# Performance work log

Hardware: AMD Instinct MI355X
Metric: run time of the kernel (lower is better)

The kernel has to match this reference:

```python
import jax, jax.numpy as jnp
import numpy as np

D_MODEL = 256
NUM_HEADS = 8
D_HEAD = D_MODEL // NUM_HEADS  # 32


def setup_inputs() -> dict:
    key = jax.random.key(0)
    ks = jax.random.split(key, 7)
    N, WH = 8, 2048
    s = 1.0 / np.sqrt(D_MODEL)
    return {
        "x": jax.random.normal(ks[0], (N, WH, D_MODEL), dtype=jnp.float32),
        "Wq": jax.random.normal(ks[1], (D_MODEL, D_MODEL), dtype=jnp.float32) * s,
        "bq": jnp.zeros((D_MODEL,), dtype=jnp.float32),
        "Wk": jax.random.normal(ks[2], (D_MODEL, D_MODEL), dtype=jnp.float32) * s,
        "bk": jnp.zeros((D_MODEL,), dtype=jnp.float32),
        "Wv": jax.random.normal(ks[3], (D_MODEL, D_MODEL), dtype=jnp.float32) * s,
        "bv": jnp.zeros((D_MODEL,), dtype=jnp.float32),
    }


def _mhsa(x, Wq, bq, Wk, bk, Wv, bv):
    N, WH, C = x.shape
    # QKV projections; reshape to (N, heads, WH, d_head)
    def split_heads(t):
        return t.reshape(N, WH, NUM_HEADS, D_HEAD).transpose(0, 2, 1, 3)
    Q = split_heads(x @ Wq + bq)
    K = split_heads(x @ Wk + bk)
    V = split_heads(x @ Wv + bv)
    # FAITHFUL to source: logits /= d_k**(-0.5)  ==  logits * sqrt(d_k)
    logits = jnp.einsum("nhqd,nhkd->nhqk", Q, K) * jnp.sqrt(jnp.float32(D_HEAD))
    attn = jax.nn.softmax(logits, axis=-1)  # dropout p=0.1 is identity in eval
    x_attn = jnp.einsum("nhqk,nhkd->nhqd", attn, V)
    x_attn = x_attn.transpose(0, 2, 1, 3).reshape(N, WH, C)
    # drop_path is identity in eval mode; residual add
    return x_attn + x


def reference(x, Wq, bq, Wk, bk, Wv, bv):
    return _mhsa(x, Wq, bq, Wk, bk, Wv, bv)
```

## Files before the change

### kernel.cpp

```cpp
#include <hip/hip_runtime.h>
#include <math.h>

#define WH 2048
#define DM 256
#define NHD 8
#define DH 32
#define NB 8

typedef __attribute__((ext_vector_type(8))) short short8;
typedef __attribute__((ext_vector_type(4))) short short4v;
typedef __attribute__((ext_vector_type(4))) float f32x4;

__device__ __forceinline__ unsigned short bf16_rn(float f) {
    unsigned u = __float_as_uint(f);
    return (unsigned short)((u + 0x8000u) >> 16);
}
__device__ __forceinline__ float bf16_to_f(unsigned short h) {
    return __uint_as_float(((unsigned)h) << 16);
}
__device__ __forceinline__ unsigned pack_bf16_rn(float f1, float f0) {
    return __builtin_amdgcn_perm(__float_as_uint(f1) + 0x8000u,
                                 __float_as_uint(f0) + 0x8000u, 0x07060302);
}
__device__ __forceinline__ void glds16(const void* g, void* l) {
    __builtin_amdgcn_global_load_lds(
        (const __attribute__((address_space(1))) unsigned int*)g,
        (__attribute__((address_space(3))) unsigned int*)l, 16, 0, 0);
}

__global__ __launch_bounds__(256) void xprep(
    const float* __restrict__ X,
    unsigned short* __restrict__ Xhi, unsigned short* __restrict__ Xlo)
{
    const size_t i = ((size_t)blockIdx.x * 256 + threadIdx.x) * 8;
    float4 a = *(const float4*)&X[i];
    float4 b = *(const float4*)&X[i + 4];
    float v[8] = {a.x, a.y, a.z, a.w, b.x, b.y, b.z, b.w};
    short8 hi, lo;
    #pragma unroll
    for (int e = 0; e < 8; e++) {
        unsigned short hb = bf16_rn(v[e]);
        hi[e] = (short)hb;
        lo[e] = (short)bf16_rn(v[e] - bf16_to_f(hb));
    }
    *(short8*)&Xhi[i] = hi;
    *(short8*)&Xlo[i] = lo;
}

__global__ __launch_bounds__(256) void wprep(
    const float* __restrict__ Wq, const float* __restrict__ Wk,
    const float* __restrict__ Wv,
    unsigned short* __restrict__ WThi, unsigned short* __restrict__ WTlo)
{
    const int z = blockIdx.y;
    const float* W = (z == 0) ? Wq : ((z == 1) ? Wk : Wv);
    const size_t zoff = (size_t)z * DM * DM;
    const int tg = blockIdx.x * 256 + threadIdx.x;
    #pragma unroll
    for (int j = 0; j < 4; j++) {
        const int f = tg + j * 4096;
        const int k  = f >> 6;
        const int n0 = (f & 63) * 4;
        float4 v = *(const float4*)&W[(size_t)k * DM + n0];
        float vv[4] = {v.x, v.y, v.z, v.w};
        #pragma unroll
        for (int i = 0; i < 4; i++) {
            unsigned short hb = bf16_rn(vv[i]);
            WThi[zoff + (size_t)(n0 + i) * DM + k] = hb;
            WTlo[zoff + (size_t)(n0 + i) * DM + k] = bf16_rn(vv[i] - bf16_to_f(hb));
        }
    }
}

__global__ __launch_bounds__(256, 1) void qkv_mfma(
    const unsigned short* __restrict__ Xhi, const unsigned short* __restrict__ Xlo,
    const unsigned short* __restrict__ WThi, const unsigned short* __restrict__ WTlo,
    const float* __restrict__ bq, const float* __restrict__ bk, const float* __restrict__ bv,
    unsigned short* __restrict__ Qhi, unsigned short* __restrict__ Qlo,
    unsigned short* __restrict__ Khi, unsigned short* __restrict__ Klo,
    unsigned short* __restrict__ Vt)
{
    __shared__ __align__(16) unsigned short arena[4 * 2 * 4096];

    const int z = blockIdx.z;
    const float* bias = (z == 0) ? bq : ((z == 1) ? bk : bv);
    const size_t zoff = (size_t)z * DM * DM;

    const int tid  = threadIdx.x;
    const int w    = tid >> 6;
    const int lane = tid & 63;
    const int col  = lane & 15;
    const int quad = lane >> 4;
    const int wr = w >> 1, wc = w & 1;
    const int bm = blockIdx.x * 128;
    const int bn = blockIdx.y * 128;

    const int perm16 = (((lane & 3) ^ ((lane >> 3) & 3))) * 16;
    const char* glane;
    if (w == 0)      glane = (const char*)Xhi + (size_t)(bm + (lane >> 2)) * 512 + perm16;
    else if (w == 1) glane = (const char*)Xlo + (size_t)(bm + (lane >> 2)) * 512 + perm16;
    else if (w == 2) glane = (const char*)(WThi + zoff) + (size_t)(bn + (lane >> 2)) * 512 + perm16;
    else             glane = (const char*)(WTlo + zoff) + (size_t)(bn + (lane >> 2)) * 512 + perm16;

    auto issue = [&](int kb, int b) {
        const char* g0 = glane + (size_t)kb * 64;
        unsigned short* l0 = &arena[w * 8192 + b * 4096];
        #pragma unroll
        for (int g = 0; g < 8; g++)
            glds16(g0 + (size_t)g * 8192, l0 + g * 512);
    };

    f32x4 acc[4][4];
    #pragma unroll
    for (int mi = 0; mi < 4; mi++)
        #pragma unroll
        for (int ni = 0; ni < 4; ni++) acc[mi][ni] = (f32x4){0.f, 0.f, 0.f, 0.f};

    const int sw = (col >> 1) & 3;
    const int fO = (quad ^ sw) * 8;

    issue(0, 0);
    __syncthreads();
    for (int kb = 0; kb < 8; kb++) {
        const int b = kb & 1;
        if (kb < 7) issue(kb + 1, b ^ 1);

        short8 ah[4], al[4], bh[4], bl[4];
        #pragma unroll
        for (int mi = 0; mi < 4; mi++) {
            const int ro = (wr * 64 + mi * 16 + col) * 32 + fO;
            ah[mi] = *(const short8*)&arena[        b * 4096 + ro];
            al[mi] = *(const short8*)&arena[ 8192 + b * 4096 + ro];
        }
        #pragma unroll
        for (int ni = 0; ni < 4; ni++) {
            const int no = (wc * 64 + ni * 16 + col) * 32 + fO;
            bh[ni] = *(const short8*)&arena[16384 + b * 4096 + no];
            bl[ni] = *(const short8*)&arena[24576 + b * 4096 + no];
        }
        #pragma unroll
        for (int mi = 0; mi < 4; mi++)
            #pragma unroll
            for (int ni = 0; ni < 4; ni++) {
                acc[mi][ni] = __builtin_amdgcn_mfma_f32_16x16x32_bf16(al[mi], bh[ni], acc[mi][ni], 0, 0, 0);
                acc[mi][ni] = __builtin_amdgcn_mfma_f32_16x16x32_bf16(ah[mi], bl[ni], acc[mi][ni], 0, 0, 0);
                acc[mi][ni] = __builtin_amdgcn_mfma_f32_16x16x32_bf16(ah[mi], bh[ni], acc[mi][ni], 0, 0, 0);
            }
        __syncthreads();
    }

    unsigned* Tp = (unsigned*)arena;
    const int n   = bm >> 11;
    const int wqb = bm & (WH - 1);
    const float qsc = (z == 0) ? 8.1611159f : 1.0f;

    #pragma unroll
    for (int p = 0; p < 2; p++) {
        if (wr == p) {
            #pragma unroll
            for (int mi = 0; mi < 4; mi++)
                #pragma unroll
                for (int ni = 0; ni < 4; ni++) {
                    const int lc = wc * 64 + ni * 16 + col;
                    const float bb = bias[bn + lc];
                    #pragma unroll
                    for (int r = 0; r < 4; r++) {
                        float v = (acc[mi][ni][r] + bb) * qsc;
                        unsigned short hb = bf16_rn(v);
                        unsigned short lb = bf16_rn(v - bf16_to_f(hb));
                        Tp[(mi * 16 + quad * 4 + r) * 132 + lc] =
                            (unsigned)hb | ((unsigned)lb << 16);
                    }
                }
        }
        __syncthreads();
        if (z == 2) {
            const int c = tid >> 1, half = tid & 1;
            const int coln = bn + c, h = coln >> 5, d = coln & 31;
            const int tI = (wqb + p * 64 + half * 32) >> 5;
            unsigned short* dst =
                &Vt[(((size_t)(n * NHD + h) * 64 + tI) * 32 + d) * 32];
            unsigned hi[16];
            #pragma unroll
            for (int jj = 0; jj < 16; jj++) {
                unsigned u0 = Tp[(half * 32 + 2 * jj    ) * 132 + c];
                unsigned u1 = Tp[(half * 32 + 2 * jj + 1) * 132 + c];
                hi[jj] = __builtin_amdgcn_perm(u1, u0, 0x05040100);
            }
            #pragma unroll
            for (int s = 0; s < 4; s++)
                *(uint4*)&dst[s * 8] = make_uint4(hi[4*s], hi[4*s+1], hi[4*s+2], hi[4*s+3]);
        } else {
            const int lr = tid >> 2, seg = tid & 3;
            const int coln0 = bn + seg * 32, h = coln0 >> 5;
            const size_t off = ((size_t)((n * NHD + h) * WH) + wqb + p * 64 + lr) * DH;
            unsigned short* Thi = (z == 0) ? Qhi : Khi;
            unsigned short* Tlo = (z == 0) ? Qlo : Klo;
            #pragma unroll
            for (int s = 0; s < 4; s++) {
                unsigned u[8], hi[4], lo[4];
                *(uint4*)&u[0] = *(uint4*)&Tp[lr * 132 + seg * 32 + s * 8];
                *(uint4*)&u[4] = *(uint4*)&Tp[lr * 132 + seg * 32 + s * 8 + 4];
                #pragma unroll
                for (int jj = 0; jj < 4; jj++) {
                    hi[jj] = __builtin_amdgcn_perm(u[2*jj+1], u[2*jj], 0x05040100);
                    lo[jj] = __builtin_amdgcn_perm(u[2*jj+1], u[2*jj], 0x07060302);
                }
                *(uint4*)&Thi[off + s * 8] = make_uint4(hi[0], hi[1], hi[2], hi[3]);
                *(uint4*)&Tlo[off + s * 8] = make_uint4(lo[0], lo[1], lo[2], lo[3]);
            }
        }
        __syncthreads();
    }
}

__global__ __launch_bounds__(256, 4) void attn(
    const unsigned short* __restrict__ Qhi, const unsigned short* __restrict__ Qlo,
    const unsigned short* __restrict__ Khi, const unsigned short* __restrict__ Klo,
    const unsigned short* __restrict__ Vt,  const float* __restrict__ X,
    float* __restrict__ Out)
{
    __shared__ __align__(16) unsigned short Kh[2][1024];
    __shared__ __align__(16) unsigned short Kl[2][1024];
    __shared__ __align__(16) unsigned short Vv[2][1024];

    const int tid  = threadIdx.x;
    const int w    = tid >> 6;
    const int lane = tid & 63;
    const int col  = lane & 15;
    const int quad = lane >> 4;
    const int nh   = blockIdx.y;
    const int q0   = blockIdx.x * 128;
    const size_t base = (size_t)nh * WH * DH;

    short8 qh[2], ql[2];
    #pragma unroll
    for (int f = 0; f < 2; f++) {
        const int qrow = q0 + f * 64 + w * 16 + col;
        qh[f] = *(const short8*)&Qhi[base + (size_t)qrow * DH + quad * 8];
        ql[f] = *(const short8*)&Qlo[base + (size_t)qrow * DH + quad * 8];
    }

    f32x4 ot00 = {0.f,0.f,0.f,0.f}, ot01 = {0.f,0.f,0.f,0.f};
    f32x4 ot10 = {0.f,0.f,0.f,0.f}, ot11 = {0.f,0.f,0.f,0.f};
    float mr0 = -INFINITY, mr1 = -INFINITY, lr0 = 0.f, lr1 = 0.f;

    const size_t toff = (size_t)(lane >> 2) * 64 + (((lane & 3) ^ ((lane >> 3) & 3))) * 16;
    const char* gb;
    unsigned short *ld0, *ld1;
    if (w == 0)      { gb = (const char*)(Khi + base);        ld0 = &Kh[0][0];   ld1 = &Kh[1][0];   }
    else if (w == 1) { gb = (const char*)(Klo + base);        ld0 = &Kl[0][0];   ld1 = &Kl[1][0];   }
    else if (w == 2) { gb = (const char*)(Vt  + base);        ld0 = &Vv[0][0];   ld1 = &Vv[1][0];   }
    else             { gb = (const char*)(Vt  + base) + 1024; ld0 = &Vv[0][512]; ld1 = &Vv[1][512]; }
    gb += toff;

    auto issue = [&](int t, unsigned short* ld) {
        const char* g = gb + (size_t)t * 2048;
        glds16(g, ld);
        if (w < 2) glds16(g + 1024, ld + 512);
    };

    const int sw  = (col >> 1) & 3;
    const int kO0 = col * 32 + (quad ^ sw) * 8;
    const int vO0 = col * 32 + ((quad >> 1) ^ sw) * 8 + (quad & 1) * 4;
    const int vO1 = col * 32 + ((2 + (quad >> 1)) ^ sw) * 8 + (quad & 1) * 4;

    auto body = [&](int b) {
        const short8 kh0 = *(const short8*)&Kh[b][kO0];
        const short8 kh1 = *(const short8*)&Kh[b][kO0 + 512];
        const short8 kl0 = *(const short8*)&Kl[b][kO0];
        const short8 kl1 = *(const short8*)&Kl[b][kO0 + 512];
        const short4v va00 = *(const short4v*)&Vv[b][vO0];
        const short4v va01 = *(const short4v*)&Vv[b][vO1];
        const short4v va10 = *(const short4v*)&Vv[b][vO0 + 512];
        const short4v va11 = *(const short4v*)&Vv[b][vO1 + 512];

        #pragma unroll
        for (int f = 0; f < 2; f++) {
            f32x4 s0 = {0.f,0.f,0.f,0.f}, s1 = {0.f,0.f,0.f,0.f};
            s0 = __builtin_amdgcn_mfma_f32_16x16x32_bf16(kh0, ql[f], s0, 0, 0, 0);
            s0 = __builtin_amdgcn_mfma_f32_16x16x32_bf16(kl0, qh[f], s0, 0, 0, 0);
            s0 = __builtin_amdgcn_mfma_f32_16x16x32_bf16(kh0, qh[f], s0, 0, 0, 0);
            s1 = __builtin_amdgcn_mfma_f32_16x16x32_bf16(kh1, ql[f], s1, 0, 0, 0);
            s1 = __builtin_amdgcn_mfma_f32_16x16x32_bf16(kl1, qh[f], s1, 0, 0, 0);
            s1 = __builtin_amdgcn_mfma_f32_16x16x32_bf16(kh1, qh[f], s1, 0, 0, 0);

            float mx = fmaxf(fmaxf(fmaxf(s0[0], s0[1]), fmaxf(s0[2], s0[3])),
                             fmaxf(fmaxf(s1[0], s1[1]), fmaxf(s1[2], s1[3])));
            mx = fmaxf(mx, __shfl_xor(mx, 16));
            mx = fmaxf(mx, __shfl_xor(mx, 32));
            float& mrf = f ? mr1 : mr0;
            float& lrf = f ? lr1 : lr0;
            const float mnew  = fmaxf(mrf, mx);
            const float alpha = __builtin_amdgcn_exp2f(mrf - mnew);

            float p0[4], p1[4], ps = 0.f;
            #pragma unroll
            for (int r = 0; r < 4; r++) {
                p0[r] = __builtin_amdgcn_exp2f(s0[r] - mnew); ps += p0[r];
                p1[r] = __builtin_amdgcn_exp2f(s1[r] - mnew); ps += p1[r];
            }
            ps += __shfl_xor(ps, 16);
            ps += __shfl_xor(ps, 32);
            lrf = lrf * alpha + ps;
            mrf = mnew;

            union { short4v v; unsigned u[2]; } Pb0, Pb1;
            Pb0.u[0] = pack_bf16_rn(p0[1], p0[0]);
            Pb0.u[1] = pack_bf16_rn(p0[3], p0[2]);
            Pb1.u[0] = pack_bf16_rn(p1[1], p1[0]);
            Pb1.u[1] = pack_bf16_rn(p1[3], p1[2]);

            f32x4& o0 = f ? ot10 : ot00;
            f32x4& o1 = f ? ot11 : ot01;
            #pragma unroll
            for (int r = 0; r < 4; r++) { o0[r] *= alpha; o1[r] *= alpha; }
            o0 = __builtin_amdgcn_mfma_f32_16x16x16bf16_1k(va00, Pb0.v, o0, 0, 0, 0);
            o0 = __builtin_amdgcn_mfma_f32_16x16x16bf16_1k(va01, Pb1.v, o0, 0, 0, 0);
            o1 = __builtin_amdgcn_mfma_f32_16x16x16bf16_1k(va10, Pb0.v, o1, 0, 0, 0);
            o1 = __builtin_amdgcn_mfma_f32_16x16x16bf16_1k(va11, Pb1.v, o1, 0, 0, 0);
        }
    };

    issue(0, ld0);
    __syncthreads();
    for (int kt2 = 0; kt2 < 32; kt2++) {
        issue(2 * kt2 + 1, ld1);
        body(0);
        __syncthreads();
        if (kt2 < 31) issue(2 * kt2 + 2, ld0);
        body(1);
        __syncthreads();
    }

    const int n = nh >> 3, h = nh & 7;
    #pragma unroll
    for (int f = 0; f < 2; f++) {
        const float inv = 1.f / (f ? lr1 : lr0);
        const f32x4& o0 = f ? ot10 : ot00;
        const f32x4& o1 = f ? ot11 : ot01;
        const int qrow = q0 + f * 64 + w * 16 + col;
        const size_t a0 = ((size_t)n * WH + qrow) * DM + h * DH + quad * 4;
        float4 x0 = *(const float4*)&X[a0];
        float4 y0;
        y0.x = o0[0] * inv + x0.x;
        y0.y = o0[1] * inv + x0.y;
        y0.z = o0[2] * inv + x0.z;
        y0.w = o0[3] * inv + x0.w;
        *(float4*)&Out[a0] = y0;
        float4 x1 = *(const float4*)&X[a0 + 16];
        float4 y1;
        y1.x = o1[0] * inv + x1.x;
        y1.y = o1[1] * inv + x1.y;
        y1.z = o1[2] * inv + x1.z;
        y1.w = o1[3] * inv + x1.w;
        *(float4*)&Out[a0 + 16] = y1;
    }
}

extern "C" void kernel_launch(void* const* d_in, const int* in_sizes, int n_in,
                              void* d_out, int out_size, void* d_ws, size_t ws_size,
                              hipStream_t stream) {
    const float* x  = (const float*)d_in[0];
    const float* Wq = (const float*)d_in[1];
    const float* bq = (const float*)d_in[2];
    const float* Wk = (const float*)d_in[3];
    const float* bk = (const float*)d_in[4];
    const float* Wv = (const float*)d_in[5];
    const float* bv = (const float*)d_in[6];
    float* out = (float*)d_out;

    const size_t elems = (size_t)NB * WH * DM;
    unsigned short* Qhi  = (unsigned short*)d_ws;
    unsigned short* Qlo  = Qhi + elems;
    unsigned short* Khi  = Qlo + elems;
    unsigned short* Klo  = Khi + elems;
    unsigned short* Vt   = Klo + elems;
    unsigned short* WThi = Vt  + elems;
    unsigned short* WTlo = WThi + (size_t)3 * DM * DM;

    unsigned short* Xhi = (unsigned short*)d_out;
    unsigned short* Xlo = Xhi + elems;

    xprep<<<2048, 256, 0, stream>>>(x, Xhi, Xlo);

    dim3 gw(16, 3);
    wprep<<<gw, 256, 0, stream>>>(Wq, Wk, Wv, WThi, WTlo);

    dim3 gg(128, 2, 3);
    qkv_mfma<<<gg, 256, 0, stream>>>(Xhi, Xlo, WThi, WTlo, bq, bk, bv,
                                     Qhi, Qlo, Khi, Klo, Vt);

    dim3 ga(WH / 128, NB * NHD);
    attn<<<ga, 256, 0, stream>>>(Qhi, Qlo, Khi, Klo, Vt, x, out);
}
```

Measured before the change: 232.6 us.

## Pack K/V tiles into contiguous blobs and process 64 keys per attention step

The QKV projection now writes K hi/lo and transposed V for each 64-key tile into one contiguous 12 KB blob per head, and X/W are pre-laid out in k-chunked blocks so GEMM tile loads are contiguous. The attention kernel loads each blob with three async LDS copies per wave and processes 64 keys per iteration instead of 32, halving loop iterations and barriers. Row-sum shuffles are deferred to the epilogue. In exchange it uses more LDS, holds more registers per iteration, and adds a new XOR swizzle for V reads.

```diff
diff --git a/kernel.cpp b/kernel.cpp
--- a/kernel.cpp
+++ b/kernel.cpp
@@ -33,6 +33,9 @@
     unsigned short* __restrict__ Xhi, unsigned short* __restrict__ Xlo)
 {
     const size_t i = ((size_t)blockIdx.x * 256 + threadIdx.x) * 8;
+    const int row = (int)(i >> 8);
+    const int k   = (int)(i & 255);
+    const size_t dst = ((size_t)(k >> 5) * 16384 + row) * 32 + (k & 31);
     float4 a = *(const float4*)&X[i];
     float4 b = *(const float4*)&X[i + 4];
     float v[8] = {a.x, a.y, a.z, a.w, b.x, b.y, b.z, b.w};
@@ -43,8 +46,8 @@
         hi[e] = (short)hb;
         lo[e] = (short)bf16_rn(v[e] - bf16_to_f(hb));
     }
-    *(short8*)&Xhi[i] = hi;
-    *(short8*)&Xlo[i] = lo;
+    *(short8*)&Xhi[dst] = hi;
+    *(short8*)&Xlo[dst] = lo;
 }
 
 __global__ __launch_bounds__(256) void wprep(
@@ -66,8 +69,9 @@
         #pragma unroll
         for (int i = 0; i < 4; i++) {
             unsigned short hb = bf16_rn(vv[i]);
-            WThi[zoff + (size_t)(n0 + i) * DM + k] = hb;
-            WTlo[zoff + (size_t)(n0 + i) * DM + k] = bf16_rn(vv[i] - bf16_to_f(hb));
+            const size_t dst = zoff + ((size_t)(k >> 5) * 256 + n0 + i) * 32 + (k & 31);
+            WThi[dst] = hb;
+            WTlo[dst] = bf16_rn(vv[i] - bf16_to_f(hb));
         }
     }
 }
@@ -77,8 +81,7 @@
     const unsigned short* __restrict__ WThi, const unsigned short* __restrict__ WTlo,
     const float* __restrict__ bq, const float* __restrict__ bk, const float* __restrict__ bv,
     unsigned short* __restrict__ Qhi, unsigned short* __restrict__ Qlo,
-    unsigned short* __restrict__ Khi, unsigned short* __restrict__ Klo,
-    unsigned short* __restrict__ Vt)
+    unsigned short* __restrict__ KV)
 {
     __shared__ __align__(16) unsigned short arena[4 * 2 * 4096];
 
@@ -96,18 +99,18 @@
     const int bn = blockIdx.y * 128;
 
     const int perm16 = (((lane & 3) ^ ((lane >> 3) & 3))) * 16;
-    const char* glane;
-    if (w == 0)      glane = (const char*)Xhi + (size_t)(bm + (lane >> 2)) * 512 + perm16;
-    else if (w == 1) glane = (const char*)Xlo + (size_t)(bm + (lane >> 2)) * 512 + perm16;
-    else if (w == 2) glane = (const char*)(WThi + zoff) + (size_t)(bn + (lane >> 2)) * 512 + perm16;
-    else             glane = (const char*)(WTlo + zoff) + (size_t)(bn + (lane >> 2)) * 512 + perm16;
+    const char* glane; size_t kstr;
+    if (w == 0)      { glane = (const char*)Xhi + (size_t)(bm + (lane >> 2)) * 64 + perm16; kstr = (size_t)16384 * 64; }
+    else if (w == 1) { glane = (const char*)Xlo + (size_t)(bm + (lane >> 2)) * 64 + perm16; kstr = (size_t)16384 * 64; }
+    else if (w == 2) { glane = (const char*)(WThi + zoff) + (size_t)(bn + (lane >> 2)) * 64 + perm16; kstr = 256 * 64; }
+    else             { glane = (const char*)(WTlo + zoff) + (size_t)(bn + (lane >> 2)) * 64 + perm16; kstr = 256 * 64; }
 
     auto issue = [&](int kb, int b) {
-        const char* g0 = glane + (size_t)kb * 64;
+        const char* g0 = glane + (size_t)kb * kstr;
         unsigned short* l0 = &arena[w * 8192 + b * 4096];
         #pragma unroll
         for (int g = 0; g < 8; g++)
-            glds16(g0 + (size_t)g * 8192, l0 + g * 512);
+            glds16(g0 + (size_t)g * 1024, l0 + g * 512);
     };
 
     f32x4 acc[4][4];
@@ -177,9 +180,10 @@
         if (z == 2) {
             const int c = tid >> 1, half = tid & 1;
             const int coln = bn + c, h = coln >> 5, d = coln & 31;
-            const int tI = (wqb + p * 64 + half * 32) >> 5;
+            const int key0 = wqb + p * 64 + half * 32;
+            const int t = key0 >> 6, k6 = key0 & 63;
             unsigned short* dst =
-                &Vt[(((size_t)(n * NHD + h) * 64 + tI) * 32 + d) * 32];
+                &KV[(((size_t)(n * NHD + h) * 32 + t) * 6144) + 4096 + d * 64 + k6];
             unsigned hi[16];
             #pragma unroll
             for (int jj = 0; jj < 16; jj++) {
@@ -190,12 +194,13 @@
             #pragma unroll
             for (int s = 0; s < 4; s++)
                 *(uint4*)&dst[s * 8] = make_uint4(hi[4*s], hi[4*s+1], hi[4*s+2], hi[4*s+3]);
-        } else {
+        } else if (z == 1) {
             const int lr = tid >> 2, seg = tid & 3;
-            const int coln0 = bn + seg * 32, h = coln0 >> 5;
-            const size_t off = ((size_t)((n * NHD + h) * WH) + wqb + p * 64 + lr) * DH;
-            unsigned short* Thi = (z == 0) ? Qhi : Khi;
-            unsigned short* Tlo = (z == 0) ? Qlo : Klo;
+            const int h = (bn + seg * 32) >> 5;
+            const int key = wqb + p * 64 + lr;
+            const int t = key >> 6, k6 = key & 63;
+            unsigned short* blobK =
+                &KV[(((size_t)(n * NHD + h) * 32 + t) * 6144) + k6 * 32];
             #pragma unroll
             for (int s = 0; s < 4; s++) {
                 unsigned u[8], hi[4], lo[4];
@@ -206,8 +211,25 @@
                     hi[jj] = __builtin_amdgcn_perm(u[2*jj+1], u[2*jj], 0x05040100);
                     lo[jj] = __builtin_amdgcn_perm(u[2*jj+1], u[2*jj], 0x07060302);
                 }
-                *(uint4*)&Thi[off + s * 8] = make_uint4(hi[0], hi[1], hi[2], hi[3]);
-                *(uint4*)&Tlo[off + s * 8] = make_uint4(lo[0], lo[1], lo[2], lo[3]);
+                *(uint4*)&blobK[s * 8]        = make_uint4(hi[0], hi[1], hi[2], hi[3]);
+                *(uint4*)&blobK[2048 + s * 8] = make_uint4(lo[0], lo[1], lo[2], lo[3]);
+            }
+        } else {
+            const int lr = tid >> 2, seg = tid & 3;
+            const int h = (bn + seg * 32) >> 5;
+            const size_t off = ((size_t)((n * NHD + h) * WH) + wqb + p * 64 + lr) * DH;
+            #pragma unroll
+            for (int s = 0; s < 4; s++) {
+                unsigned u[8], hi[4], lo[4];
+                *(uint4*)&u[0] = *(uint4*)&Tp[lr * 132 + seg * 32 + s * 8];
+                *(uint4*)&u[4] = *(uint4*)&Tp[lr * 132 + seg * 32 + s * 8 + 4];
+                #pragma unroll
+                for (int jj = 0; jj < 4; jj++) {
+                    hi[jj] = __builtin_amdgcn_perm(u[2*jj+1], u[2*jj], 0x05040100);
+                    lo[jj] = __builtin_amdgcn_perm(u[2*jj+1], u[2*jj], 0x07060302);
+                }
+                *(uint4*)&Qhi[off + s * 8] = make_uint4(hi[0], hi[1], hi[2], hi[3]);
+                *(uint4*)&Qlo[off + s * 8] = make_uint4(lo[0], lo[1], lo[2], lo[3]);
             }
         }
         __syncthreads();
@@ -216,13 +238,10 @@
 
 __global__ __launch_bounds__(256, 4) void attn(
     const unsigned short* __restrict__ Qhi, const unsigned short* __restrict__ Qlo,
-    const unsigned short* __restrict__ Khi, const unsigned short* __restrict__ Klo,
-    const unsigned short* __restrict__ Vt,  const float* __restrict__ X,
+    const unsigned short* __restrict__ KV,  const float* __restrict__ X,
     float* __restrict__ Out)
 {
-    __shared__ __align__(16) unsigned short Kh[2][1024];
-    __shared__ __align__(16) unsigned short Kl[2][1024];
-    __shared__ __align__(16) unsigned short Vv[2][1024];
+    __shared__ __align__(16) unsigned short B[2][6144];
 
     const int tid  = threadIdx.x;
     const int w    = tid >> 6;
@@ -231,62 +250,74 @@
     const int quad = lane >> 4;
     const int nh   = blockIdx.y;
     const int q0   = blockIdx.x * 128;
-    const size_t base = (size_t)nh * WH * DH;
+    const size_t qbase = (size_t)nh * WH * DH;
+    const char* blob = (const char*)(KV + (size_t)nh * 196608);
 
     short8 qh[2], ql[2];
     #pragma unroll
     for (int f = 0; f < 2; f++) {
         const int qrow = q0 + f * 64 + w * 16 + col;
-        qh[f] = *(const short8*)&Qhi[base + (size_t)qrow * DH + quad * 8];
-        ql[f] = *(const short8*)&Qlo[base + (size_t)qrow * DH + quad * 8];
-    }
-
-    f32x4 ot00 = {0.f,0.f,0.f,0.f}, ot01 = {0.f,0.f,0.f,0.f};
-    f32x4 ot10 = {0.f,0.f,0.f,0.f}, ot11 = {0.f,0.f,0.f,0.f};
+        qh[f] = *(const short8*)&Qhi[qbase + (size_t)qrow * DH + quad * 8];
+        ql[f] = *(const short8*)&Qlo[qbase + (size_t)qrow * DH + quad * 8];
+    }
+
+    f32x4 o00 = {0.f,0.f,0.f,0.f}, o01 = {0.f,0.f,0.f,0.f};
+    f32x4 o10 = {0.f,0.f,0.f,0.f}, o11 = {0.f,0.f,0.f,0.f};
     float mr0 = -INFINITY, mr1 = -INFINITY, lr0 = 0.f, lr1 = 0.f;
 
-    const size_t toff = (size_t)(lane >> 2) * 64 + (((lane & 3) ^ ((lane >> 3) & 3))) * 16;
-    const char* gb;
-    unsigned short *ld0, *ld1;
-    if (w == 0)      { gb = (const char*)(Khi + base);        ld0 = &Kh[0][0];   ld1 = &Kh[1][0];   }
-    else if (w == 1) { gb = (const char*)(Klo + base);        ld0 = &Kl[0][0];   ld1 = &Kl[1][0];   }
-    else if (w == 2) { gb = (const char*)(Vt  + base);        ld0 = &Vv[0][0];   ld1 = &Vv[1][0];   }
-    else             { gb = (const char*)(Vt  + base) + 1024; ld0 = &Vv[0][512]; ld1 = &Vv[1][512]; }
-    gb += toff;
-
-    auto issue = [&](int t, unsigned short* ld) {
-        const char* g = gb + (size_t)t * 2048;
-        glds16(g, ld);
-        if (w < 2) glds16(g + 1024, ld + 512);
+    const char* gseg[3];
+    int loseg[3];
+    #pragma unroll
+    for (int j = 0; j < 3; j++) {
+        const int s = w * 3 + j;
+        int loff;
+        if (s < 8) loff = (lane >> 2) * 64  + (((lane & 3) ^ ((lane >> 3) & 3)) << 4);
+        else       loff = (lane >> 3) * 128 + (((lane & 7) ^ ((lane >> 3) & 7)) << 4);
+        gseg[j] = blob + s * 1024 + loff;
+        loseg[j] = s * 512;
+    }
+
+    auto issue = [&](int t, int b) {
+        #pragma unroll
+        for (int j = 0; j < 3; j++)
+            glds16(gseg[j] + (size_t)t * 12288, &B[b][loseg[j]]);
     };
 
-    const int sw  = (col >> 1) & 3;
-    const int kO0 = col * 32 + (quad ^ sw) * 8;
-    const int vO0 = col * 32 + ((quad >> 1) ^ sw) * 8 + (quad & 1) * 4;
-    const int vO1 = col * 32 + ((2 + (quad >> 1)) ^ sw) * 8 + (quad & 1) * 4;
+    const int sw = (col >> 1) & 3;
 
     auto body = [&](int b) {
-        const short8 kh0 = *(const short8*)&Kh[b][kO0];
-        const short8 kh1 = *(const short8*)&Kh[b][kO0 + 512];
-        const short8 kl0 = *(const short8*)&Kl[b][kO0];
-        const short8 kl1 = *(const short8*)&Kl[b][kO0 + 512];
-        const short4v va00 = *(const short4v*)&Vv[b][vO0];
-        const short4v va01 = *(const short4v*)&Vv[b][vO1];
-        const short4v va10 = *(const short4v*)&Vv[b][vO0 + 512];
-        const short4v va11 = *(const short4v*)&Vv[b][vO1 + 512];
-
+        const unsigned short* Bp = &B[b][0];
+        short8 kh[4], kl[4];
+        #pragma unroll
+        for (int kc = 0; kc < 4; kc++) {
+            const int ro = (col + kc * 16) * 32 + (quad ^ sw) * 8;
+            kh[kc] = *(const short8*)&Bp[ro];
+            kl[kc] = *(const short8*)&Bp[2048 + ro];
+        }
+        short4v va[4][2];
+        #pragma unroll
+        for (int kc = 0; kc < 4; kc++) {
+            const int cl = kc * 2 + (quad >> 1);
+            const int co = ((cl ^ (col & 7)) << 3) + (quad & 1) * 4;
+            va[kc][0] = *(const short4v*)&Bp[4096 + (col     ) * 64 + co];
+            va[kc][1] = *(const short4v*)&Bp[4096 + (col + 16) * 64 + co];
+        }
         #pragma unroll
         for (int f = 0; f < 2; f++) {
-            f32x4 s0 = {0.f,0.f,0.f,0.f}, s1 = {0.f,0.f,0.f,0.f};
-            s0 = __builtin_amdgcn_mfma_f32_16x16x32_bf16(kh0, ql[f], s0, 0, 0, 0);
-            s0 = __builtin_amdgcn_mfma_f32_16x16x32_bf16(kl0, qh[f], s0, 0, 0, 0);
-            s0 = __builtin_amdgcn_mfma_f32_16x16x32_bf16(kh0, qh[f], s0, 0, 0, 0);
-            s1 = __builtin_amdgcn_mfma_f32_16x16x32_bf16(kh1, ql[f], s1, 0, 0, 0);
-            s1 = __builtin_amdgcn_mfma_f32_16x16x32_bf16(kl1, qh[f], s1, 0, 0, 0);
-            s1 = __builtin_amdgcn_mfma_f32_16x16x32_bf16(kh1, qh[f], s1, 0, 0, 0);
-
-            float mx = fmaxf(fmaxf(fmaxf(s0[0], s0[1]), fmaxf(s0[2], s0[3])),
-                             fmaxf(fmaxf(s1[0], s1[1]), fmaxf(s1[2], s1[3])));
+            f32x4 s[4];
+            #pragma unroll
+            for (int kc = 0; kc < 4; kc++) {
+                f32x4 a = {0.f, 0.f, 0.f, 0.f};
+                a = __builtin_amdgcn_mfma_f32_16x16x32_bf16(kh[kc], ql[f], a, 0, 0, 0);
+                a = __builtin_amdgcn_mfma_f32_16x16x32_bf16(kl[kc], qh[f], a, 0, 0, 0);
+                a = __builtin_amdgcn_mfma_f32_16x16x32_bf16(kh[kc], qh[f], a, 0, 0, 0);
+                s[kc] = a;
+            }
+            float mx = s[0][0];
+            #pragma unroll
+            for (int kc = 0; kc < 4; kc++)
+                #pragma unroll
+                for (int r = 0; r < 4; r++) mx = fmaxf(mx, s[kc][r]);
             mx = fmaxf(mx, __shfl_xor(mx, 16));
             mx = fmaxf(mx, __shfl_xor(mx, 32));
             float& mrf = f ? mr1 : mr0;
@@ -294,41 +325,45 @@
             const float mnew  = fmaxf(mrf, mx);
             const float alpha = __builtin_amdgcn_exp2f(mrf - mnew);
 
-            float p0[4], p1[4], ps = 0.f;
-            #pragma unroll
-            for (int r = 0; r < 4; r++) {
-                p0[r] = __builtin_amdgcn_exp2f(s0[r] - mnew); ps += p0[r];
-                p1[r] = __builtin_amdgcn_exp2f(s1[r] - mnew); ps += p1[r];
-            }
-            ps += __shfl_xor(ps, 16);
-            ps += __shfl_xor(ps, 32);
+            float ps = 0.f;
+            #pragma unroll
+            for (int kc = 0; kc < 4; kc++)
+                #pragma unroll
+                for (int r = 0; r < 4; r++) {
+                    s[kc][r] = __builtin_amdgcn_exp2f(s[kc][r] - mnew);
+                    ps += s[kc][r];
+                }
             lrf = lrf * alpha + ps;
             mrf = mnew;
 
-            union { short4v v; unsigned u[2]; } Pb0, Pb1;
-            Pb0.u[0] = pack_bf16_rn(p0[1], p0[0]);
-            Pb0.u[1] = pack_bf16_rn(p0[3], p0[2]);
-            Pb1.u[0] = pack_bf16_rn(p1[1], p1[0]);
-            Pb1.u[1] = pack_bf16_rn(p1[3], p1[2]);
-
-            f32x4& o0 = f ? ot10 : ot00;
-            f32x4& o1 = f ? ot11 : ot01;
-            #pragma unroll
-            for (int r = 0; r < 4; r++) { o0[r] *= alpha; o1[r] *= alpha; }
-            o0 = __builtin_amdgcn_mfma_f32_16x16x16bf16_1k(va00, Pb0.v, o0, 0, 0, 0);
-            o0 = __builtin_amdgcn_mfma_f32_16x16x16bf16_1k(va01, Pb1.v, o0, 0, 0, 0);
-            o1 = __builtin_amdgcn_mfma_f32_16x16x16bf16_1k(va10, Pb0.v, o1, 0, 0, 0);
-            o1 = __builtin_amdgcn_mfma_f32_16x16x16bf16_1k(va11, Pb1.v, o1, 0, 0, 0);
+            short4v pb[4];
+            #pragma unroll
+            for (int kc = 0; kc < 4; kc++) {
+                union { short4v v; unsigned u[2]; } P;
+                P.u[0] = pack_bf16_rn(s[kc][1], s[kc][0]);
+                P.u[1] = pack_bf16_rn(s[kc][3], s[kc][2]);
+                pb[kc] = P.v;
+            }
+
+            f32x4& a0 = f ? o10 : o00;
+            f32x4& a1 = f ? o11 : o01;
+            #pragma unroll
+            for (int r = 0; r < 4; r++) { a0[r] *= alpha; a1[r] *= alpha; }
+            #pragma unroll
+            for (int kc = 0; kc < 4; kc++) {
+                a0 = __builtin_amdgcn_mfma_f32_16x16x16bf16_1k(va[kc][0], pb[kc], a0, 0, 0, 0);
+                a1 = __builtin_amdgcn_mfma_f32_16x16x16bf16_1k(va[kc][1], pb[kc], a1, 0, 0, 0);
+            }
         }
     };
 
-    issue(0, ld0);
+    issue(0, 0);
     __syncthreads();
-    for (int kt2 = 0; kt2 < 32; kt2++) {
-        issue(2 * kt2 + 1, ld1);
+    for (int t2 = 0; t2 < 16; t2++) {
+        issue(2 * t2 + 1, 1);
         body(0);
         __syncthreads();
-        if (kt2 < 31) issue(2 * kt2 + 2, ld0);
+        if (t2 < 15) issue(2 * t2 + 2, 0);
         body(1);
         __syncthreads();
     }
@@ -336,25 +371,28 @@
     const int n = nh >> 3, h = nh & 7;
     #pragma unroll
     for (int f = 0; f < 2; f++) {
-        const float inv = 1.f / (f ? lr1 : lr0);
-        const f32x4& o0 = f ? ot10 : ot00;
-        const f32x4& o1 = f ? ot11 : ot01;
+        float l = f ? lr1 : lr0;
+        l += __shfl_xor(l, 16);
+        l += __shfl_xor(l, 32);
+        const float inv = 1.f / l;
+        const f32x4& a0 = f ? o10 : o00;
+        const f32x4& a1 = f ? o11 : o01;
         const int qrow = q0 + f * 64 + w * 16 + col;
-        const size_t a0 = ((size_t)n * WH + qrow) * DM + h * DH + quad * 4;
-        float4 x0 = *(const float4*)&X[a0];
+        const size_t a = ((size_t)n * WH + qrow) * DM + h * DH + quad * 4;
+        float4 x0 = *(const float4*)&X[a];
         float4 y0;
-        y0.x = o0[0] * inv + x0.x;
-        y0.y = o0[1] * inv + x0.y;
-        y0.z = o0[2] * inv + x0.z;
-        y0.w = o0[3] * inv + x0.w;
-        *(float4*)&Out[a0] = y0;
-        float4 x1 = *(const float4*)&X[a0 + 16];
+        y0.x = a0[0] * inv + x0.x;
+        y0.y = a0[1] * inv + x0.y;
+        y0.z = a0[2] * inv + x0.z;
+        y0.w = a0[3] * inv + x0.w;
+        *(float4*)&Out[a] = y0;
+        float4 x1 = *(const float4*)&X[a + 16];
         float4 y1;
-        y1.x = o1[0] * inv + x1.x;
-        y1.y = o1[1] * inv + x1.y;
-        y1.z = o1[2] * inv + x1.z;
-        y1.w = o1[3] * inv + x1.w;
-        *(float4*)&Out[a0 + 16] = y1;
+        y1.x = a1[0] * inv + x1.x;
+        y1.y = a1[1] * inv + x1.y;
+        y1.z = a1[2] * inv + x1.z;
+        y1.w = a1[3] * inv + x1.w;
+        *(float4*)&Out[a + 16] = y1;
     }
 }
 
@@ -373,10 +411,8 @@
     const size_t elems = (size_t)NB * WH * DM;
     unsigned short* Qhi  = (unsigned short*)d_ws;
     unsigned short* Qlo  = Qhi + elems;
-    unsigned short* Khi  = Qlo + elems;
-    unsigned short* Klo  = Khi + elems;
-    unsigned short* Vt   = Klo + elems;
-    unsigned short* WThi = Vt  + elems;
+    unsigned short* KV   = Qlo + elems;
+    unsigned short* WThi = KV  + (size_t)64 * 32 * 6144;
     unsigned short* WTlo = WThi + (size_t)3 * DM * DM;
 
     unsigned short* Xhi = (unsigned short*)d_out;
@@ -389,8 +425,8 @@
 
     dim3 gg(128, 2, 3);
     qkv_mfma<<<gg, 256, 0, stream>>>(Xhi, Xlo, WThi, WTlo, bq, bk, bv,
-                                     Qhi, Qlo, Khi, Klo, Vt);
+                                     Qhi, Qlo, KV);
 
     dim3 ga(WH / 128, NB * NHD);
-    attn<<<ga, 256, 0, stream>>>(Qhi, Qlo, Khi, Klo, Vt, x, out);
-}
+    attn<<<ga, 256, 0, stream>>>(Qhi, Qlo, KV, x, out);
+}
```

Result: faster. 217.8 us (-6.4%).
